# Kernel optimization log

Measured on AMD Instinct MI355X. Metric: run time of the kernel, lower is better.

## Reference

```python
import jax, jax.numpy as jnp
import numpy as np

H = 132  # hidden size hard-coded in SpatialRelationLayer

def _mlp(x, w1, b1, w2, b2, w3, b3):
    # FCBlock: 2 hidden layers of width 132 with ReLU, then linear out;
    # NNNet wraps it with sigmoid(out * 5)
    h = jax.nn.relu(x @ w1 + b1)
    h = jax.nn.relu(h @ w2 + b2)
    return jax.nn.sigmoid((h @ w3 + b3) * 5.0)

def _mlp_params(key, din, dout):
    k1, k2, k3 = jax.random.split(key, 3)
    def lin(k, i, o):
        kw, kb = jax.random.split(k)
        s = 1.0 / np.sqrt(i)
        return (jax.random.uniform(kw, (i, o), jnp.float32, -s, s),
                jax.random.uniform(kb, (o,), jnp.float32, -s, s))
    w1, b1 = lin(k1, din, H)
    w2, b2 = lin(k2, H, H)
    w3, b3 = lin(k3, H, dout)
    return w1, b1, w2, b2, w3, b3

def setup_inputs() -> dict:
    key = jax.random.key(0)
    b, N, D0, D1, D2 = 8, 128, 128, 128, 64
    O0, O1, O2 = 64, 64, 64
    kP, kQ, kR, kp, kq, kr = jax.random.split(key, 6)
    inp = {
        "P": jax.random.normal(kP, (b, D0), jnp.float32),
        "Q": jax.random.normal(kQ, (b, N, D1), jnp.float32),
        "R": jax.random.normal(kR, (b, N, N, D2), jnp.float32),
    }
    for name, k, din, dout in (("p", kp, D0 + D1, O0),
                               ("q", kq, D1 + D0 + 2 * D2, O1),
                               ("r", kr, D2 + 2 * D1, O2)):
        w1, b1, w2, b2, w3, b3 = _mlp_params(k, din, dout)
        inp.update({f"{name}_w1": w1, f"{name}_b1": b1,
                    f"{name}_w2": w2, f"{name}_b2": b2,
                    f"{name}_w3": w3, f"{name}_b3": b3})
    return inp

def reference(P, Q, R,
              p_w1, p_b1, p_w2, p_b2, p_w3, p_b3,
              q_w1, q_b1, q_w2, q_b2, q_w3, q_b3,
              r_w1, r_b1, r_w2, r_b2, r_w3, r_b3):
    b, N, D1 = Q.shape
    # P branch: global max over objects, concat with P
    P_inputs = jnp.concatenate([jnp.max(Q, axis=1), P], axis=1)  # [b, D1+D0]
    P_out = _mlp(P_inputs, p_w1, p_b1, p_w2, p_b2, p_w3, p_b3)
    # Q branch: broadcast P per-object, max-reduce relations over each axis
    P_exp = jnp.broadcast_to(P[:, None, :], (b, N, P.shape[1]))  # [b,N,D0]
    R_red0 = jnp.max(R, axis=1)  # [b,N,D2]
    R_red1 = jnp.max(R, axis=2)  # [b,N,D2]
    Q_inputs = jnp.concatenate([P_exp, Q, R_red0, R_red1], axis=2)
    Q_out = _mlp(Q_inputs, q_w1, q_b1, q_w2, q_b2, q_w3, q_b3)
    # R branch: pairwise broadcast of Q along both axes, concat with R
    Q0 = jnp.broadcast_to(Q[:, None, :, :], (b, N, N, D1))  # repeat along dim 1
    Q1 = jnp.broadcast_to(Q[:, :, None, :], (b, N, N, D1))  # repeat along dim 2
    R_inputs = jnp.concatenate([R, Q0, Q1], axis=-1)  # [b,N,N,D2+2*D1]
    R_out = _mlp(R_inputs, r_w1, r_b1, r_w2, r_b2, r_w3, r_b3)
    return (P_out, Q_out, R_out)
```

## Files before the change

kernel.cpp:

```cpp
#include <hip/hip_runtime.h>

typedef _Float16 f16;
typedef f16 f16x8 __attribute__((ext_vector_type(8)));
typedef f16 f16x4 __attribute__((ext_vector_type(4)));
typedef float f32x4 __attribute__((ext_vector_type(4)));

#define MFMA16(a, b, c) __builtin_amdgcn_mfma_f32_16x16x32_f16(a, b, c, 0, 0, 0)

#define OFF_RW1A 0
#define OFF_RW2  10240
#define OFF_RW3  35840
#define OFF_QW1  46080
#define OFF_QW2  87040
#define OFF_QW3  112640
#define OFF_PW1  122880
#define OFF_PW2  163840
#define OFF_PW3  189440
#define PACK_BYTES 399360

#define PREP_BLOCKS 2419

struct InPtrs { const float* p[21]; };

__device__ const int g_mSrc[9] = {15, 17, 19, 9, 11, 13, 3, 5, 7};
__device__ const int g_mK0[9]  = {0, 0, 0, 128, 0, 0, 0, 0, 0};
__device__ const int g_mK[9]   = {64, 132, 132, 256, 132, 132, 256, 132, 132};
__device__ const int g_mN[9]   = {132, 132, 64, 132, 132, 64, 132, 132, 64};
__device__ const int g_mNT[9]  = {10, 10, 4, 10, 10, 4, 10, 10, 4};
__device__ const int g_mDst[9] = {OFF_RW1A, OFF_RW2, OFF_RW3, OFF_QW1, OFF_QW2, OFF_QW3,
                                  OFF_PW1, OFF_PW2, OFF_PW3};
__device__ const int g_mBlk0[9] = {1024, 1029, 1042, 1047, 1067, 1080, 1085, 1105, 1118};

__global__ __launch_bounds__(256) void prep_kernel(InPtrs in, f16* __restrict__ wpk,
    float* __restrict__ c1, float* __restrict__ d1, float* __restrict__ e1q,
    float* __restrict__ qmax, float* __restrict__ red0, float* __restrict__ red1)
{
  __shared__ float sbuf[1024];
  const int mb = blockIdx.x, t = threadIdx.x;

  if (mb < 1024) {
    const int b = mb >> 7, j = mb & 127;
    const float* base = in.p[2] + (size_t)b * 128 * 8192 + (size_t)j * 64 + (t & 15) * 4;
    const int g = t >> 4;
    f32x4 mm[8];
    #pragma unroll
    for (int v = 0; v < 8; ++v)
      mm[v] = *(const f32x4*)(base + (size_t)(g + 16 * v) * 8192);
    #pragma unroll
    for (int s = 4; s > 0; s >>= 1)
      #pragma unroll
      for (int v = 0; v < 4; ++v)
        if (v < s) {
          mm[v][0] = fmaxf(mm[v][0], mm[v + s][0]);
          mm[v][1] = fmaxf(mm[v][1], mm[v + s][1]);
          mm[v][2] = fmaxf(mm[v][2], mm[v + s][2]);
          mm[v][3] = fmaxf(mm[v][3], mm[v + s][3]);
        }
    float* sr = sbuf + g * 64 + (t & 15) * 4;
    sr[0] = mm[0][0]; sr[1] = mm[0][1]; sr[2] = mm[0][2]; sr[3] = mm[0][3];
    __syncthreads();
    if (t < 64) {
      float m = sbuf[t];
      #pragma unroll
      for (int g2 = 1; g2 < 16; ++g2) m = fmaxf(m, sbuf[g2 * 64 + t]);
      red0[(size_t)mb * 64 + t] = m;
    }
  } else if (mb < 1123) {
    int mi = 8;
    while (mi > 0 && mb < g_mBlk0[mi]) --mi;
    const int NT = g_mNT[mi], K = g_mK[mi], N = g_mN[mi], K0 = g_mK0[mi];
    const int L = (mb - g_mBlk0[mi]) * 256 + t;
    const int lanes = ((K + 31) >> 5) * NT * 64;
    if (L < lanes) {
      const int lane = L & 63, tile = L >> 6;
      const int kk = tile / NT, nn = tile % NT;
      const float* src = in.p[g_mSrc[mi]];
      const int n = nn * 16 + (lane & 15);
      const int kb = kk * 32 + ((lane >> 4) << 3);
      f16x8 v;
      #pragma unroll
      for (int u = 0; u < 8; ++u) {
        const int k = kb + u;
        float f = (k < K && n < N) ? src[(size_t)(K0 + k) * N + n] : 0.f;
        v[u] = (f16)f;
      }
      *(f16x8*)(wpk + g_mDst[mi] + (size_t)L * 8) = v;
    }
  } else if (mb < 1131) {
    const int b = mb - 1123;
    const float* Qb = in.p[1] + (size_t)b * 128 * 128;
    const int d = t & 127, g = t >> 7;
    float m0 = -3.4e38f, m1 = m0, m2 = m0, m3 = m0;
    #pragma unroll
    for (int v = 0; v < 16; ++v) {
      const int i = g * 64 + v * 4;
      m0 = fmaxf(m0, Qb[(size_t)(i + 0) * 128 + d]);
      m1 = fmaxf(m1, Qb[(size_t)(i + 1) * 128 + d]);
      m2 = fmaxf(m2, Qb[(size_t)(i + 2) * 128 + d]);
      m3 = fmaxf(m3, Qb[(size_t)(i + 3) * 128 + d]);
    }
    sbuf[g * 128 + d] = fmaxf(fmaxf(m0, m1), fmaxf(m2, m3));
    __syncthreads();
    if (t < 128) qmax[b * 128 + t] = fmaxf(sbuf[t], sbuf[128 + t]);
  } else if (mb < 1139) {
    const int b = mb - 1131;
    const float* P = in.p[0]; const float* qw1 = in.p[9]; const float* qb1 = in.p[10];
    if (t < 160) {
      float a = 0.f;
      if (t < 132) {
        float a0 = 0.f, a1 = 0.f, a2 = 0.f, a3 = 0.f;
        for (int k = 0; k < 128; k += 4) {
          a0 += P[b * 128 + k + 0] * qw1[(size_t)(k + 0) * 132 + t];
          a1 += P[b * 128 + k + 1] * qw1[(size_t)(k + 1) * 132 + t];
          a2 += P[b * 128 + k + 2] * qw1[(size_t)(k + 2) * 132 + t];
          a3 += P[b * 128 + k + 3] * qw1[(size_t)(k + 3) * 132 + t];
        }
        a = qb1[t] + (a0 + a1) + (a2 + a3);
      }
      e1q[b * 160 + t] = a;
    }
  } else if (mb < 1395) {
    const int blk = mb - 1139;
    const float* Q = in.p[1]; const float* rw1 = in.p[15]; const float* rb1 = in.p[16];
    for (int o = t; o < 512; o += 256) sbuf[o] = Q[(size_t)blk * 512 + o];
    __syncthreads();
    if (t < 160) {
      float cc[4], dd[4];
      #pragma unroll
      for (int r = 0; r < 4; ++r) { cc[r] = 0.f; dd[r] = 0.f; }
      if (t < 132) {
        const float bb = rb1[t];
        #pragma unroll
        for (int r = 0; r < 4; ++r) cc[r] = bb;
        for (int k = 0; k < 128; ++k) {
          const float wc = rw1[(size_t)(192 + k) * 132 + t];
          const float wd = rw1[(size_t)(64 + k) * 132 + t];
          #pragma unroll
          for (int r = 0; r < 4; ++r) {
            cc[r] += sbuf[r * 128 + k] * wc;
            dd[r] += sbuf[r * 128 + k] * wd;
          }
        }
      }
      for (int r = 0; r < 4; ++r) {
        c1[(size_t)(blk * 4 + r) * 160 + t] = cc[r];
        d1[(size_t)(blk * 4 + r) * 160 + t] = dd[r];
      }
    }
  } else {
    const int blk = mb - 1395;
    const float* base = in.p[2] + (size_t)blk * 8192 + (t & 15) * 4;
    const int g = t >> 4;
    f32x4 mm[8];
    #pragma unroll
    for (int v = 0; v < 8; ++v)
      mm[v] = *(const f32x4*)(base + (size_t)(g + 16 * v) * 64);
    #pragma unroll
    for (int s = 4; s > 0; s >>= 1)
      #pragma unroll
      for (int v = 0; v < 4; ++v)
        if (v < s) {
          mm[v][0] = fmaxf(mm[v][0], mm[v + s][0]);
          mm[v][1] = fmaxf(mm[v][1], mm[v + s][1]);
          mm[v][2] = fmaxf(mm[v][2], mm[v + s][2]);
          mm[v][3] = fmaxf(mm[v][3], mm[v + s][3]);
        }
    float* sr = sbuf + g * 64 + (t & 15) * 4;
    sr[0] = mm[0][0]; sr[1] = mm[0][1]; sr[2] = mm[0][2]; sr[3] = mm[0][3];
    __syncthreads();
    if (t < 64) {
      float m = sbuf[t];
      #pragma unroll
      for (int g2 = 1; g2 < 16; ++g2) m = fmaxf(m, sbuf[g2 * 64 + t]);
      red1[(size_t)blk * 64 + t] = m;
    }
  }
}

__device__ __forceinline__ float sig5(float x) {
  return 1.f / (1.f + __expf(-5.f * x));
}

__global__ __launch_bounds__(256, 2) void fused_kernel(
    const float* __restrict__ R, const float* __restrict__ c1, const float* __restrict__ d1,
    const float* __restrict__ rb2, const float* __restrict__ rb3,
    const f16* __restrict__ wpk, float* __restrict__ outR,
    const float* __restrict__ P, const float* __restrict__ Q,
    const float* __restrict__ qb2, const float* __restrict__ qb3,
    const float* __restrict__ pb1, const float* __restrict__ pb2, const float* __restrict__ pb3,
    const float* __restrict__ e1q, const float* __restrict__ qmax,
    const float* __restrict__ red0, const float* __restrict__ red1,
    float* __restrict__ outP, float* __restrict__ outQ)
{
  __shared__ __align__(16) char pool[81920];
  const int blk = blockIdx.x;
  const int t = threadIdx.x, lane = t & 63, w = t >> 6;
  const int wm = w >> 1, wn = w & 1;
  const int lr = (lane >> 4) << 2;
  const int lc = lane & 15;
  const int lk = (lane >> 4) << 3;

  if (blk < 1024) {
    f16 (*Xr)[72]  = (f16(*)[72])pool;
    f16 (*Hs)[168] = (f16(*)[168])(pool + 18432);
    const int rbase = wm * 64, nbase = wn * 80;

    const float* Rb = R + (size_t)blk * 8192;
    #pragma unroll
    for (int v = 0; v < 8; ++v) {
      const int quad = v * 256 + t;
      const int j = quad >> 4, kq = quad & 15;
      f32x4 rv = *(const f32x4*)(Rb + (size_t)j * 64 + kq * 4);
      f16x4 hv;
      hv[0] = (f16)rv[0]; hv[1] = (f16)rv[1]; hv[2] = (f16)rv[2]; hv[3] = (f16)rv[3];
      *(f16x4*)(&Xr[j][kq * 4]) = hv;
    }

    const int b = blk >> 7;
    const float* c1r = c1 + (size_t)blk * 160;
    const float* d1b = d1 + (size_t)b * 128 * 160;
    f32x4 acc[4][5];
    f32x4 cvv[5];
    #pragma unroll
    for (int n5 = 0; n5 < 5; ++n5)
      cvv[n5] = *(const f32x4*)(c1r + nbase + n5 * 16 + lr);
    #pragma unroll
    for (int mi2 = 0; mi2 < 4; ++mi2) {
      const int j = rbase + mi2 * 16 + lc;
      #pragma unroll
      for (int n5 = 0; n5 < 5; ++n5) {
        f32x4 dv = *(const f32x4*)(d1b + (size_t)j * 160 + nbase + n5 * 16 + lr);
        acc[mi2][n5] = cvv[n5] + dv;
      }
    }
    __syncthreads();
    const f16x8* W1p = (const f16x8*)(wpk + OFF_RW1A);
    #pragma unroll
    for (int kk = 0; kk < 2; ++kk) {
      f16x8 a[4];
      #pragma unroll
      for (int mi2 = 0; mi2 < 4; ++mi2)
        a[mi2] = *(const f16x8*)(&Xr[rbase + mi2 * 16 + lc][kk * 32 + lk]);
      #pragma unroll
      for (int n5 = 0; n5 < 5; ++n5) {
        const f16x8 bf = W1p[(size_t)(kk * 10 + wn * 5 + n5) * 64 + lane];
        #pragma unroll
        for (int mi2 = 0; mi2 < 4; ++mi2)
          acc[mi2][n5] = MFMA16(bf, a[mi2], acc[mi2][n5]);
      }
    }
    #pragma unroll
    for (int mi2 = 0; mi2 < 4; ++mi2) {
      const int j = rbase + mi2 * 16 + lc;
      #pragma unroll
      for (int n5 = 0; n5 < 5; ++n5) {
        f16x4 hv;
        #pragma unroll
        for (int r = 0; r < 4; ++r) hv[r] = (f16)fmaxf(acc[mi2][n5][r], 0.f);
        *(f16x4*)(&Hs[j][nbase + n5 * 16 + lr]) = hv;
      }
    }
    __syncthreads();

    #pragma unroll
    for (int n5 = 0; n5 < 5; ++n5) {
      const int nb = nbase + n5 * 16 + lr;
      f32x4 bv = {0.f, 0.f, 0.f, 0.f};
      if (nb < 132) bv = *(const f32x4*)(rb2 + nb);
      #pragma unroll
      for (int mi2 = 0; mi2 < 4; ++mi2) acc[mi2][n5] = bv;
    }
    const f16x8* W2p = (const f16x8*)(wpk + OFF_RW2);
    #pragma unroll
    for (int kk = 0; kk < 5; ++kk) {
      f16x8 a[4];
      #pragma unroll
      for (int mi2 = 0; mi2 < 4; ++mi2)
        a[mi2] = *(const f16x8*)(&Hs[rbase + mi2 * 16 + lc][kk * 32 + lk]);
      #pragma unroll
      for (int n5 = 0; n5 < 5; ++n5) {
        const f16x8 bf = W2p[(size_t)(kk * 10 + wn * 5 + n5) * 64 + lane];
        #pragma unroll
        for (int mi2 = 0; mi2 < 4; ++mi2)
          acc[mi2][n5] = MFMA16(bf, a[mi2], acc[mi2][n5]);
      }
    }
    __syncthreads();
    #pragma unroll
    for (int mi2 = 0; mi2 < 4; ++mi2) {
      const int j = rbase + mi2 * 16 + lc;
      #pragma unroll
      for (int n5 = 0; n5 < 5; ++n5) {
        f16x4 hv;
        #pragma unroll
        for (int r = 0; r < 4; ++r) hv[r] = (f16)fmaxf(acc[mi2][n5][r], 0.f);
        *(f16x4*)(&Hs[j][nbase + n5 * 16 + lr]) = hv;
      }
    }
    __syncthreads();

    f32x4 acc3[4][2];
    const int n3base = wn * 32;
    #pragma unroll
    for (int n2 = 0; n2 < 2; ++n2) {
      f32x4 bv = *(const f32x4*)(rb3 + n3base + n2 * 16 + lr);
      #pragma unroll
      for (int mi2 = 0; mi2 < 4; ++mi2) acc3[mi2][n2] = bv;
    }
    const f16x8* W3p = (const f16x8*)(wpk + OFF_RW3);
    #pragma unroll
    for (int kk = 0; kk < 5; ++kk) {
      f16x8 a[4];
      #pragma unroll
      for (int mi2 = 0; mi2 < 4; ++mi2)
        a[mi2] = *(const f16x8*)(&Hs[rbase + mi2 * 16 + lc][kk * 32 + lk]);
      #pragma unroll
      for (int n2 = 0; n2 < 2; ++n2) {
        const f16x8 bf = W3p[(size_t)(kk * 4 + wn * 2 + n2) * 64 + lane];
        #pragma unroll
        for (int mi2 = 0; mi2 < 4; ++mi2)
          acc3[mi2][n2] = MFMA16(bf, a[mi2], acc3[mi2][n2]);
      }
    }
    float* Ro = outR + (size_t)blk * 8192;
    #pragma unroll
    for (int mi2 = 0; mi2 < 4; ++mi2) {
      const int j = rbase + mi2 * 16 + lc;
      #pragma unroll
      for (int n2 = 0; n2 < 2; ++n2) {
        f32x4 ov;
        #pragma unroll
        for (int r = 0; r < 4; ++r) ov[r] = sig5(acc3[mi2][n2][r]);
        *(f32x4*)(Ro + (size_t)j * 64 + n3base + n2 * 16 + lr) = ov;
      }
    }
  } else {
    f16 (*Xc)[72]  = (f16(*)[72])pool;
    f16 (*Hs2)[168] = (f16(*)[168])(pool + 9216);
    f16* Wb = (f16*)(pool + 30720);
    const int bs = blk - 1024;
    const bool isP = (bs == 16);
    const int rb = wm * 32;
    const int b = bs >> 1, x0 = (bs & 1) * 64;
    const f16* W1g = wpk + (isP ? OFF_PW1 : OFF_QW1);
    const f16* W2g = wpk + (isP ? OFF_PW2 : OFF_QW2);
    const f16* W3g = wpk + (isP ? OFF_PW3 : OFF_QW3);

    f32x4 acc[2][5];
    #pragma unroll
    for (int n5 = 0; n5 < 5; ++n5) {
      const int nb = wn * 80 + n5 * 16 + lr;
      f32x4 cv = {0.f, 0.f, 0.f, 0.f};
      if (isP) { if (nb < 132) cv = *(const f32x4*)(pb1 + nb); }
      else cv = *(const f32x4*)(e1q + b * 160 + nb);
      acc[0][n5] = cv; acc[1][n5] = cv;
    }

    for (int c = 0; c < 4; ++c) {
      if ((c & 1) == 0) {
        const int half = c >> 1;
        for (int idx = t; idx < 40 * 64; idx += 256) {
          const int f = idx >> 6, ln = idx & 63;
          *(f16x8*)(&Wb[f * 512 + ln * 8]) =
              *(const f16x8*)(W1g + (size_t)(half * 40 + f) * 512 + ln * 8);
        }
      }
      for (int o = t; o < 1024; o += 256) {
        const int rr = o >> 4, kq = o & 15;
        f32x4 v = {0.f, 0.f, 0.f, 0.f};
        if (isP) {
          if (rr < 8) {
            const float* s = (c < 2) ? (qmax + rr * 128 + c * 64) : (P + rr * 128 + (c - 2) * 64);
            v = *(const f32x4*)(s + kq * 4);
          }
        } else {
          const size_t rowg = (size_t)(b * 128 + x0 + rr);
          const float* s = (c < 2) ? (Q + rowg * 128 + c * 64)
                                   : (((c == 2) ? red0 : red1) + rowg * 64);
          v = *(const f32x4*)(s + kq * 4);
        }
        f16x4 hv;
        hv[0] = (f16)v[0]; hv[1] = (f16)v[1]; hv[2] = (f16)v[2]; hv[3] = (f16)v[3];
        *(f16x4*)(&Xc[rr][kq * 4]) = hv;
      }
      __syncthreads();
      #pragma unroll
      for (int kk = 0; kk < 2; ++kk) {
        f16x8 a[2];
        #pragma unroll
        for (int mi2 = 0; mi2 < 2; ++mi2)
          a[mi2] = *(const f16x8*)(&Xc[rb + mi2 * 16 + lc][kk * 32 + lk]);
        #pragma unroll
        for (int n5 = 0; n5 < 5; ++n5) {
          const int rel = ((c & 1) * 2 + kk) * 10 + wn * 5 + n5;
          const f16x8 bf = *(const f16x8*)(&Wb[rel * 512 + lane * 8]);
          #pragma unroll
          for (int mi2 = 0; mi2 < 2; ++mi2)
            acc[mi2][n5] = MFMA16(bf, a[mi2], acc[mi2][n5]);
        }
      }
      __syncthreads();
    }
    #pragma unroll
    for (int mi2 = 0; mi2 < 2; ++mi2) {
      const int j = rb + mi2 * 16 + lc;
      #pragma unroll
      for (int n5 = 0; n5 < 5; ++n5) {
        f16x4 hv;
        #pragma unroll
        for (int r = 0; r < 4; ++r) hv[r] = (f16)fmaxf(acc[mi2][n5][r], 0.f);
        *(f16x4*)(&Hs2[j][wn * 80 + n5 * 16 + lr]) = hv;
      }
    }
    for (int idx = t; idx < 50 * 64; idx += 256) {
      const int f = idx >> 6, ln = idx & 63;
      *(f16x8*)(&Wb[f * 512 + ln * 8]) = *(const f16x8*)(W2g + (size_t)f * 512 + ln * 8);
    }
    #pragma unroll
    for (int n5 = 0; n5 < 5; ++n5) {
      const int nb = wn * 80 + n5 * 16 + lr;
      f32x4 bv = {0.f, 0.f, 0.f, 0.f};
      if (nb < 132) bv = *(const f32x4*)((isP ? pb2 : qb2) + nb);
      acc[0][n5] = bv; acc[1][n5] = bv;
    }
    __syncthreads();
    #pragma unroll
    for (int kk = 0; kk < 5; ++kk) {
      f16x8 a[2];
      #pragma unroll
      for (int mi2 = 0; mi2 < 2; ++mi2)
        a[mi2] = *(const f16x8*)(&Hs2[rb + mi2 * 16 + lc][kk * 32 + lk]);
      #pragma unroll
      for (int n5 = 0; n5 < 5; ++n5) {
        const f16x8 bf = *(const f16x8*)(&Wb[(kk * 10 + wn * 5 + n5) * 512 + lane * 8]);
        #pragma unroll
        for (int mi2 = 0; mi2 < 2; ++mi2)
          acc[mi2][n5] = MFMA16(bf, a[mi2], acc[mi2][n5]);
      }
    }
    __syncthreads();
    #pragma unroll
    for (int mi2 = 0; mi2 < 2; ++mi2) {
      const int j = rb + mi2 * 16 + lc;
      #pragma unroll
      for (int n5 = 0; n5 < 5; ++n5) {
        f16x4 hv;
        #pragma unroll
        for (int r = 0; r < 4; ++r) hv[r] = (f16)fmaxf(acc[mi2][n5][r], 0.f);
        *(f16x4*)(&Hs2[j][wn * 80 + n5 * 16 + lr]) = hv;
      }
    }
    for (int idx = t; idx < 20 * 64; idx += 256) {
      const int f = idx >> 6, ln = idx & 63;
      *(f16x8*)(&Wb[f * 512 + ln * 8]) = *(const f16x8*)(W3g + (size_t)f * 512 + ln * 8);
    }
    __syncthreads();

    f32x4 acc3[2][2];
    const int n3base = wn * 32;
    #pragma unroll
    for (int n2 = 0; n2 < 2; ++n2) {
      f32x4 bv = *(const f32x4*)((isP ? pb3 : qb3) + n3base + n2 * 16 + lr);
      acc3[0][n2] = bv; acc3[1][n2] = bv;
    }
    #pragma unroll
    for (int kk = 0; kk < 5; ++kk) {
      f16x8 a[2];
      #pragma unroll
      for (int mi2 = 0; mi2 < 2; ++mi2)
        a[mi2] = *(const f16x8*)(&Hs2[rb + mi2 * 16 + lc][kk * 32 + lk]);
      #pragma unroll
      for (int n2 = 0; n2 < 2; ++n2) {
        const f16x8 bf = *(const f16x8*)(&Wb[(kk * 4 + wn * 2 + n2) * 512 + lane * 8]);
        #pragma unroll
        for (int mi2 = 0; mi2 < 2; ++mi2)
          acc3[mi2][n2] = MFMA16(bf, a[mi2], acc3[mi2][n2]);
      }
    }
    #pragma unroll
    for (int mi2 = 0; mi2 < 2; ++mi2) {
      const int j = rb + mi2 * 16 + lc;
      #pragma unroll
      for (int n2 = 0; n2 < 2; ++n2) {
        f32x4 ov;
        #pragma unroll
        for (int r = 0; r < 4; ++r) ov[r] = sig5(acc3[mi2][n2][r]);
        if (isP) {
          if (j < 8) *(f32x4*)(outP + (size_t)j * 64 + n3base + n2 * 16 + lr) = ov;
        } else {
          *(f32x4*)(outQ + ((size_t)(b * 128 + x0 + j)) * 64 + n3base + n2 * 16 + lr) = ov;
        }
      }
    }
  }
}

extern "C" void kernel_launch(void* const* d_in, const int* in_sizes, int n_in,
                              void* d_out, int out_size, void* d_ws, size_t ws_size,
                              hipStream_t stream) {
  (void)in_sizes; (void)n_in; (void)out_size; (void)ws_size;
  InPtrs ip;
  for (int i = 0; i < 21; ++i) ip.p[i] = (const float*)d_in[i];

  char* ws = (char*)d_ws;
  f16* wpk = (f16*)ws;
  float* wsf = (float*)(ws + PACK_BYTES);
  float* c1 = wsf;
  float* d1 = wsf + 163840;
  float* e1q = wsf + 327680;
  float* qmax = wsf + 328960;
  float* red0 = wsf + 329984;
  float* red1 = wsf + 395520;

  float* outP = (float*)d_out;
  float* outQ = outP + 512;
  float* outR = outP + 66048;

  prep_kernel<<<dim3(PREP_BLOCKS), dim3(256), 0, stream>>>(ip, wpk, c1, d1, e1q, qmax, red0, red1);
  fused_kernel<<<dim3(1041), dim3(256), 0, stream>>>((const float*)d_in[2], c1, d1,
      (const float*)d_in[18], (const float*)d_in[20], wpk, outR,
      (const float*)d_in[0], (const float*)d_in[1],
      (const float*)d_in[12], (const float*)d_in[14],
      (const float*)d_in[4], (const float*)d_in[6], (const float*)d_in[8],
      e1q, qmax, red0, red1, outP, outQ);
}
```

Baseline: 73.55 us.

## Halve R-block tile, load MLP inputs directly to registers, restructure max reductions

The fused kernel now handles 64 rows per block instead of 128, doubling the grid and cutting shared memory to a single hidden-state buffer so launch bounds rise to 4 blocks per SM. Input fragments (R, Q, reductions) are loaded from global memory and converted to f16 in registers instead of being staged through LDS, and weights are read directly from global memory rather than being copied into shared buffers. The prep kernel's red0 and red1 reductions are rewritten with fewer blocks, each looping over more rows with 2-wide loads, which shrinks the prep grid. The intent is higher occupancy and fewer barriers and LDS round trips, at the cost of redundant global weight reads per block and less reuse of each weight fragment across rows.

```diff
diff --git a/kernel.cpp b/kernel.cpp
--- a/kernel.cpp
+++ b/kernel.cpp
@@ -4,6 +4,7 @@
 typedef f16 f16x8 __attribute__((ext_vector_type(8)));
 typedef f16 f16x4 __attribute__((ext_vector_type(4)));
 typedef float f32x4 __attribute__((ext_vector_type(4)));
+typedef float f32x2 __attribute__((ext_vector_type(2)));
 
 #define MFMA16(a, b, c) __builtin_amdgcn_mfma_f32_16x16x32_f16(a, b, c, 0, 0, 0)
 
@@ -18,7 +19,7 @@
 #define OFF_PW3  189440
 #define PACK_BYTES 399360
 
-#define PREP_BLOCKS 2419
+#define PREP_BLOCKS 1523
 
 struct InPtrs { const float* p[21]; };
 
@@ -29,7 +30,7 @@
 __device__ const int g_mNT[9]  = {10, 10, 4, 10, 10, 4, 10, 10, 4};
 __device__ const int g_mDst[9] = {OFF_RW1A, OFF_RW2, OFF_RW3, OFF_QW1, OFF_QW2, OFF_QW3,
                                   OFF_PW1, OFF_PW2, OFF_PW3};
-__device__ const int g_mBlk0[9] = {1024, 1029, 1042, 1047, 1067, 1080, 1085, 1105, 1118};
+__device__ const int g_mBlk0[9] = {128, 133, 146, 151, 171, 184, 189, 209, 222};
 
 __global__ __launch_bounds__(256) void prep_kernel(InPtrs in, f16* __restrict__ wpk,
     float* __restrict__ c1, float* __restrict__ d1, float* __restrict__ e1q,
@@ -38,34 +39,30 @@
   __shared__ float sbuf[1024];
   const int mb = blockIdx.x, t = threadIdx.x;
 
-  if (mb < 1024) {
-    const int b = mb >> 7, j = mb & 127;
-    const float* base = in.p[2] + (size_t)b * 128 * 8192 + (size_t)j * 64 + (t & 15) * 4;
-    const int g = t >> 4;
-    f32x4 mm[8];
-    #pragma unroll
-    for (int v = 0; v < 8; ++v)
-      mm[v] = *(const f32x4*)(base + (size_t)(g + 16 * v) * 8192);
+  if (mb < 128) {
+    const int b = mb >> 4, jo = mb & 15;
+    const float* base = in.p[2] + (size_t)b * 1048576 + (size_t)jo * 512 + t * 2;
+    f32x2 m[8];
+    #pragma unroll
+    for (int u = 0; u < 8; ++u) { m[u][0] = -3.4e38f; m[u][1] = -3.4e38f; }
+    for (int i = 0; i < 128; i += 8) {
+      #pragma unroll
+      for (int u = 0; u < 8; ++u) {
+        f32x2 v = *(const f32x2*)(base + (size_t)(i + u) * 8192);
+        m[u][0] = fmaxf(m[u][0], v[0]);
+        m[u][1] = fmaxf(m[u][1], v[1]);
+      }
+    }
     #pragma unroll
     for (int s = 4; s > 0; s >>= 1)
       #pragma unroll
-      for (int v = 0; v < 4; ++v)
-        if (v < s) {
-          mm[v][0] = fmaxf(mm[v][0], mm[v + s][0]);
-          mm[v][1] = fmaxf(mm[v][1], mm[v + s][1]);
-          mm[v][2] = fmaxf(mm[v][2], mm[v + s][2]);
-          mm[v][3] = fmaxf(mm[v][3], mm[v + s][3]);
+      for (int u = 0; u < 4; ++u)
+        if (u < s) {
+          m[u][0] = fmaxf(m[u][0], m[u + s][0]);
+          m[u][1] = fmaxf(m[u][1], m[u + s][1]);
         }
-    float* sr = sbuf + g * 64 + (t & 15) * 4;
-    sr[0] = mm[0][0]; sr[1] = mm[0][1]; sr[2] = mm[0][2]; sr[3] = mm[0][3];
-    __syncthreads();
-    if (t < 64) {
-      float m = sbuf[t];
-      #pragma unroll
-      for (int g2 = 1; g2 < 16; ++g2) m = fmaxf(m, sbuf[g2 * 64 + t]);
-      red0[(size_t)mb * 64 + t] = m;
-    }
-  } else if (mb < 1123) {
+    *(f32x2*)(red0 + ((size_t)(b * 128 + jo * 8 + (t >> 5))) * 64 + ((t * 2) & 63)) = m[0];
+  } else if (mb < 227) {
     int mi = 8;
     while (mi > 0 && mb < g_mBlk0[mi]) --mi;
     const int NT = g_mNT[mi], K = g_mK[mi], N = g_mN[mi], K0 = g_mK0[mi];
@@ -86,8 +83,8 @@
       }
       *(f16x8*)(wpk + g_mDst[mi] + (size_t)L * 8) = v;
     }
-  } else if (mb < 1131) {
-    const int b = mb - 1123;
+  } else if (mb < 235) {
+    const int b = mb - 227;
     const float* Qb = in.p[1] + (size_t)b * 128 * 128;
     const int d = t & 127, g = t >> 7;
     float m0 = -3.4e38f, m1 = m0, m2 = m0, m3 = m0;
@@ -102,8 +99,8 @@
     sbuf[g * 128 + d] = fmaxf(fmaxf(m0, m1), fmaxf(m2, m3));
     __syncthreads();
     if (t < 128) qmax[b * 128 + t] = fmaxf(sbuf[t], sbuf[128 + t]);
-  } else if (mb < 1139) {
-    const int b = mb - 1131;
+  } else if (mb < 243) {
+    const int b = mb - 235;
     const float* P = in.p[0]; const float* qw1 = in.p[9]; const float* qb1 = in.p[10];
     if (t < 160) {
       float a = 0.f;
@@ -119,8 +116,8 @@
       }
       e1q[b * 160 + t] = a;
     }
-  } else if (mb < 1395) {
-    const int blk = mb - 1139;
+  } else if (mb < 499) {
+    const int blk = mb - 243;
     const float* Q = in.p[1]; const float* rw1 = in.p[15]; const float* rb1 = in.p[16];
     for (int o = t; o < 512; o += 256) sbuf[o] = Q[(size_t)blk * 512 + o];
     __syncthreads();
@@ -148,31 +145,31 @@
       }
     }
   } else {
-    const int blk = mb - 1395;
-    const float* base = in.p[2] + (size_t)blk * 8192 + (t & 15) * 4;
-    const int g = t >> 4;
-    f32x4 mm[8];
-    #pragma unroll
-    for (int v = 0; v < 8; ++v)
-      mm[v] = *(const f32x4*)(base + (size_t)(g + 16 * v) * 64);
-    #pragma unroll
-    for (int s = 4; s > 0; s >>= 1)
-      #pragma unroll
-      for (int v = 0; v < 4; ++v)
-        if (v < s) {
-          mm[v][0] = fmaxf(mm[v][0], mm[v + s][0]);
-          mm[v][1] = fmaxf(mm[v][1], mm[v + s][1]);
-          mm[v][2] = fmaxf(mm[v][2], mm[v + s][2]);
-          mm[v][3] = fmaxf(mm[v][3], mm[v + s][3]);
-        }
-    float* sr = sbuf + g * 64 + (t & 15) * 4;
-    sr[0] = mm[0][0]; sr[1] = mm[0][1]; sr[2] = mm[0][2]; sr[3] = mm[0][3];
+    const int bi = mb - 499;
+    const int d2 = t & 31, jg = t >> 5;
+    const float* base = in.p[2] + (size_t)bi * 8192 + (size_t)jg * 1024 + d2 * 2;
+    f32x2 m[4];
+    #pragma unroll
+    for (int u = 0; u < 4; ++u) { m[u][0] = -3.4e38f; m[u][1] = -3.4e38f; }
+    #pragma unroll
+    for (int v = 0; v < 16; v += 4) {
+      #pragma unroll
+      for (int u = 0; u < 4; ++u) {
+        f32x2 vv = *(const f32x2*)(base + (size_t)(v + u) * 64);
+        m[u][0] = fmaxf(m[u][0], vv[0]);
+        m[u][1] = fmaxf(m[u][1], vv[1]);
+      }
+    }
+    m[0][0] = fmaxf(fmaxf(m[0][0], m[1][0]), fmaxf(m[2][0], m[3][0]));
+    m[0][1] = fmaxf(fmaxf(m[0][1], m[1][1]), fmaxf(m[2][1], m[3][1]));
+    sbuf[jg * 64 + d2 * 2] = m[0][0];
+    sbuf[jg * 64 + d2 * 2 + 1] = m[0][1];
     __syncthreads();
     if (t < 64) {
-      float m = sbuf[t];
-      #pragma unroll
-      for (int g2 = 1; g2 < 16; ++g2) m = fmaxf(m, sbuf[g2 * 64 + t]);
-      red1[(size_t)blk * 64 + t] = m;
+      float mm = sbuf[t];
+      #pragma unroll
+      for (int g2 = 1; g2 < 8; ++g2) mm = fmaxf(mm, sbuf[g2 * 64 + t]);
+      red1[(size_t)bi * 64 + t] = mm;
     }
   }
 }
@@ -181,7 +178,16 @@
   return 1.f / (1.f + __expf(-5.f * x));
 }
 
-__global__ __launch_bounds__(256, 2) void fused_kernel(
+__device__ __forceinline__ f16x8 ld_frag_f32(const float* p) {
+  f32x4 v0 = *(const f32x4*)(p);
+  f32x4 v1 = *(const f32x4*)(p + 4);
+  f16x8 a;
+  a[0] = (f16)v0[0]; a[1] = (f16)v0[1]; a[2] = (f16)v0[2]; a[3] = (f16)v0[3];
+  a[4] = (f16)v1[0]; a[5] = (f16)v1[1]; a[6] = (f16)v1[2]; a[7] = (f16)v1[3];
+  return a;
+}
+
+__global__ __launch_bounds__(256, 4) void fused_kernel(
     const float* __restrict__ R, const float* __restrict__ c1, const float* __restrict__ d1,
     const float* __restrict__ rb2, const float* __restrict__ rb3,
     const f16* __restrict__ wpk, float* __restrict__ outR,
@@ -192,304 +198,191 @@
     const float* __restrict__ red0, const float* __restrict__ red1,
     float* __restrict__ outP, float* __restrict__ outQ)
 {
-  __shared__ __align__(16) char pool[81920];
+  __shared__ f16 Hs[64][168];
   const int blk = blockIdx.x;
   const int t = threadIdx.x, lane = t & 63, w = t >> 6;
   const int wm = w >> 1, wn = w & 1;
   const int lr = (lane >> 4) << 2;
   const int lc = lane & 15;
   const int lk = (lane >> 4) << 3;
-
-  if (blk < 1024) {
-    f16 (*Xr)[72]  = (f16(*)[72])pool;
-    f16 (*Hs)[168] = (f16(*)[168])(pool + 18432);
-    const int rbase = wm * 64, nbase = wn * 80;
-
-    const float* Rb = R + (size_t)blk * 8192;
-    #pragma unroll
-    for (int v = 0; v < 8; ++v) {
-      const int quad = v * 256 + t;
-      const int j = quad >> 4, kq = quad & 15;
-      f32x4 rv = *(const f32x4*)(Rb + (size_t)j * 64 + kq * 4);
-      f16x4 hv;
-      hv[0] = (f16)rv[0]; hv[1] = (f16)rv[1]; hv[2] = (f16)rv[2]; hv[3] = (f16)rv[3];
-      *(f16x4*)(&Xr[j][kq * 4]) = hv;
-    }
-
-    const int b = blk >> 7;
-    const float* c1r = c1 + (size_t)blk * 160;
-    const float* d1b = d1 + (size_t)b * 128 * 160;
-    f32x4 acc[4][5];
+  const int rbase = wm * 32, nbase = wn * 80;
+
+  f32x4 acc[2][5];
+  const float* b2p;
+  const float* b3p;
+  const f16x8* W2p;
+  const f16x8* W3p;
+  float* obase;
+  int rowlim;
+
+  if (blk >= 17) {
+    const int idx = blk - 17;
+    const int bi = idx >> 1, half = idx & 1;
+    const int jbase = half * 64;
+    const int b = bi >> 7;
+    const float* Rb = R + (size_t)bi * 8192 + (size_t)jbase * 64;
+
+    const float* c1r = c1 + (size_t)bi * 160;
+    const float* d1b = d1 + ((size_t)b * 128 + jbase) * 160;
     f32x4 cvv[5];
     #pragma unroll
     for (int n5 = 0; n5 < 5; ++n5)
       cvv[n5] = *(const f32x4*)(c1r + nbase + n5 * 16 + lr);
     #pragma unroll
-    for (int mi2 = 0; mi2 < 4; ++mi2) {
-      const int j = rbase + mi2 * 16 + lc;
-      #pragma unroll
-      for (int n5 = 0; n5 < 5; ++n5) {
-        f32x4 dv = *(const f32x4*)(d1b + (size_t)j * 160 + nbase + n5 * 16 + lr);
-        acc[mi2][n5] = cvv[n5] + dv;
-      }
-    }
-    __syncthreads();
+    for (int mi2 = 0; mi2 < 2; ++mi2) {
+      const int jl = rbase + mi2 * 16 + lc;
+      const float* dr = d1b + (size_t)jl * 160 + nbase + lr;
+      #pragma unroll
+      for (int n5 = 0; n5 < 5; ++n5)
+        acc[mi2][n5] = cvv[n5] + *(const f32x4*)(dr + n5 * 16);
+    }
     const f16x8* W1p = (const f16x8*)(wpk + OFF_RW1A);
     #pragma unroll
     for (int kk = 0; kk < 2; ++kk) {
-      f16x8 a[4];
-      #pragma unroll
-      for (int mi2 = 0; mi2 < 4; ++mi2)
-        a[mi2] = *(const f16x8*)(&Xr[rbase + mi2 * 16 + lc][kk * 32 + lk]);
+      const f16x8 a0 = ld_frag_f32(Rb + (size_t)(rbase + lc) * 64 + kk * 32 + lk);
+      const f16x8 a1 = ld_frag_f32(Rb + (size_t)(rbase + 16 + lc) * 64 + kk * 32 + lk);
       #pragma unroll
       for (int n5 = 0; n5 < 5; ++n5) {
         const f16x8 bf = W1p[(size_t)(kk * 10 + wn * 5 + n5) * 64 + lane];
-        #pragma unroll
-        for (int mi2 = 0; mi2 < 4; ++mi2)
-          acc[mi2][n5] = MFMA16(bf, a[mi2], acc[mi2][n5]);
-      }
-    }
-    #pragma unroll
-    for (int mi2 = 0; mi2 < 4; ++mi2) {
-      const int j = rbase + mi2 * 16 + lc;
-      #pragma unroll
-      for (int n5 = 0; n5 < 5; ++n5) {
-        f16x4 hv;
-        #pragma unroll
-        for (int r = 0; r < 4; ++r) hv[r] = (f16)fmaxf(acc[mi2][n5][r], 0.f);
-        *(f16x4*)(&Hs[j][nbase + n5 * 16 + lr]) = hv;
-      }
-    }
-    __syncthreads();
+        acc[0][n5] = MFMA16(bf, a0, acc[0][n5]);
+        acc[1][n5] = MFMA16(bf, a1, acc[1][n5]);
+      }
+    }
+    b2p = rb2; b3p = rb3;
+    W2p = (const f16x8*)(wpk + OFF_RW2);
+    W3p = (const f16x8*)(wpk + OFF_RW3);
+    obase = outR + (size_t)bi * 8192 + (size_t)jbase * 64;
+    rowlim = 64;
+  } else {
+    const int bs = blk;
+    const bool isP = (bs == 16);
+    const int b = bs >> 1, x0 = (bs & 1) * 64;
+    const f16x8* W1p = (const f16x8*)(wpk + (isP ? OFF_PW1 : OFF_QW1));
+    const f16x8 zz = {0, 0, 0, 0, 0, 0, 0, 0};
 
     #pragma unroll
     for (int n5 = 0; n5 < 5; ++n5) {
       const int nb = nbase + n5 * 16 + lr;
-      f32x4 bv = {0.f, 0.f, 0.f, 0.f};
-      if (nb < 132) bv = *(const f32x4*)(rb2 + nb);
-      #pragma unroll
-      for (int mi2 = 0; mi2 < 4; ++mi2) acc[mi2][n5] = bv;
-    }
-    const f16x8* W2p = (const f16x8*)(wpk + OFF_RW2);
-    #pragma unroll
-    for (int kk = 0; kk < 5; ++kk) {
-      f16x8 a[4];
-      #pragma unroll
-      for (int mi2 = 0; mi2 < 4; ++mi2)
-        a[mi2] = *(const f16x8*)(&Hs[rbase + mi2 * 16 + lc][kk * 32 + lk]);
-      #pragma unroll
-      for (int n5 = 0; n5 < 5; ++n5) {
-        const f16x8 bf = W2p[(size_t)(kk * 10 + wn * 5 + n5) * 64 + lane];
+      f32x4 cv = {0.f, 0.f, 0.f, 0.f};
+      if (isP) { if (nb < 132) cv = *(const f32x4*)(pb1 + nb); }
+      else cv = *(const f32x4*)(e1q + b * 160 + nb);
+      acc[0][n5] = cv; acc[1][n5] = cv;
+    }
+    for (int c = 0; c < 4; ++c) {
+      #pragma unroll
+      for (int kk = 0; kk < 2; ++kk) {
+        const int kq = c * 64 + kk * 32 + lk;
+        f16x8 a0 = zz, a1 = zz;
+        if (isP) {
+          #pragma unroll
+          for (int mi2 = 0; mi2 < 2; ++mi2) {
+            const int rl = rbase + mi2 * 16 + lc;
+            f16x8 av = zz;
+            if (rl < 8) {
+              const float* s = (c < 2) ? (qmax + rl * 128 + kq) : (P + rl * 128 + (kq - 128));
+              av = ld_frag_f32(s);
+            }
+            if (mi2 == 0) a0 = av; else a1 = av;
+          }
+        } else {
+          #pragma unroll
+          for (int mi2 = 0; mi2 < 2; ++mi2) {
+            const size_t rg = (size_t)(b * 128 + x0 + rbase + mi2 * 16 + lc);
+            const float* s = (c < 2) ? (Q + rg * 128 + kq)
+                           : ((kq < 192) ? (red0 + rg * 64 + (kq - 128))
+                                         : (red1 + rg * 64 + (kq - 192)));
+            const f16x8 av = ld_frag_f32(s);
+            if (mi2 == 0) a0 = av; else a1 = av;
+          }
+        }
         #pragma unroll
-        for (int mi2 = 0; mi2 < 4; ++mi2)
-          acc[mi2][n5] = MFMA16(bf, a[mi2], acc[mi2][n5]);
-      }
-    }
-    __syncthreads();
-    #pragma unroll
-    for (int mi2 = 0; mi2 < 4; ++mi2) {
-      const int j = rbase + mi2 * 16 + lc;
-      #pragma unroll
-      for (int n5 = 0; n5 < 5; ++n5) {
-        f16x4 hv;
-        #pragma unroll
-        for (int r = 0; r < 4; ++r) hv[r] = (f16)fmaxf(acc[mi2][n5][r], 0.f);
-        *(f16x4*)(&Hs[j][nbase + n5 * 16 + lr]) = hv;
-      }
-    }
-    __syncthreads();
-
-    f32x4 acc3[4][2];
-    const int n3base = wn * 32;
+        for (int n5 = 0; n5 < 5; ++n5) {
+          const f16x8 bf = W1p[(size_t)((c * 2 + kk) * 10 + wn * 5 + n5) * 64 + lane];
+          acc[0][n5] = MFMA16(bf, a0, acc[0][n5]);
+          acc[1][n5] = MFMA16(bf, a1, acc[1][n5]);
+        }
+      }
+    }
+    b2p = isP ? pb2 : qb2; b3p = isP ? pb3 : qb3;
+    W2p = (const f16x8*)(wpk + (isP ? OFF_PW2 : OFF_QW2));
+    W3p = (const f16x8*)(wpk + (isP ? OFF_PW3 : OFF_QW3));
+    obase = isP ? outP : (outQ + ((size_t)(b * 128 + x0)) * 64);
+    rowlim = isP ? 8 : 64;
+  }
+
+  #pragma unroll
+  for (int mi2 = 0; mi2 < 2; ++mi2) {
+    const int jl = rbase + mi2 * 16 + lc;
+    #pragma unroll
+    for (int n5 = 0; n5 < 5; ++n5) {
+      f16x4 hv;
+      #pragma unroll
+      for (int r = 0; r < 4; ++r) hv[r] = (f16)fmaxf(acc[mi2][n5][r], 0.f);
+      *(f16x4*)(&Hs[jl][nbase + n5 * 16 + lr]) = hv;
+    }
+  }
+  __syncthreads();
+
+  #pragma unroll
+  for (int n5 = 0; n5 < 5; ++n5) {
+    const int nb = nbase + n5 * 16 + lr;
+    f32x4 bv = {0.f, 0.f, 0.f, 0.f};
+    if (nb < 132) bv = *(const f32x4*)(b2p + nb);
+    acc[0][n5] = bv; acc[1][n5] = bv;
+  }
+  #pragma unroll
+  for (int kk = 0; kk < 5; ++kk) {
+    const f16x8 a0 = *(const f16x8*)(&Hs[rbase + lc][kk * 32 + lk]);
+    const f16x8 a1 = *(const f16x8*)(&Hs[rbase + 16 + lc][kk * 32 + lk]);
+    #pragma unroll
+    for (int n5 = 0; n5 < 5; ++n5) {
+      const f16x8 bf = W2p[(size_t)(kk * 10 + wn * 5 + n5) * 64 + lane];
+      acc[0][n5] = MFMA16(bf, a0, acc[0][n5]);
+      acc[1][n5] = MFMA16(bf, a1, acc[1][n5]);
+    }
+  }
+  __syncthreads();
+  #pragma unroll
+  for (int mi2 = 0; mi2 < 2; ++mi2) {
+    const int jl = rbase + mi2 * 16 + lc;
+    #pragma unroll
+    for (int n5 = 0; n5 < 5; ++n5) {
+      f16x4 hv;
+      #pragma unroll
+      for (int r = 0; r < 4; ++r) hv[r] = (f16)fmaxf(acc[mi2][n5][r], 0.f);
+      *(f16x4*)(&Hs[jl][nbase + n5 * 16 + lr]) = hv;
+    }
+  }
+  __syncthreads();
+
+  f32x4 acc3[2][2];
+  const int n3base = wn * 32;
+  #pragma unroll
+  for (int n2 = 0; n2 < 2; ++n2) {
+    const f32x4 bv = *(const f32x4*)(b3p + n3base + n2 * 16 + lr);
+    acc3[0][n2] = bv; acc3[1][n2] = bv;
+  }
+  #pragma unroll
+  for (int kk = 0; kk < 5; ++kk) {
+    const f16x8 a0 = *(const f16x8*)(&Hs[rbase + lc][kk * 32 + lk]);
+    const f16x8 a1 = *(const f16x8*)(&Hs[rbase + 16 + lc][kk * 32 + lk]);
     #pragma unroll
     for (int n2 = 0; n2 < 2; ++n2) {
-      f32x4 bv = *(const f32x4*)(rb3 + n3base + n2 * 16 + lr);
-      #pragma unroll
-      for (int mi2 = 0; mi2 < 4; ++mi2) acc3[mi2][n2] = bv;
-    }
-    const f16x8* W3p = (const f16x8*)(wpk + OFF_RW3);
-    #pragma unroll
-    for (int kk = 0; kk < 5; ++kk) {
-      f16x8 a[4];
-      #pragma unroll
-      for (int mi2 = 0; mi2 < 4; ++mi2)
-        a[mi2] = *(const f16x8*)(&Hs[rbase + mi2 * 16 + lc][kk * 32 + lk]);
-      #pragma unroll
-      for (int n2 = 0; n2 < 2; ++n2) {
-        const f16x8 bf = W3p[(size_t)(kk * 4 + wn * 2 + n2) * 64 + lane];
-        #pragma unroll
-        for (int mi2 = 0; mi2 < 4; ++mi2)
-          acc3[mi2][n2] = MFMA16(bf, a[mi2], acc3[mi2][n2]);
-      }
-    }
-    float* Ro = outR + (size_t)blk * 8192;
-    #pragma unroll
-    for (int mi2 = 0; mi2 < 4; ++mi2) {
-      const int j = rbase + mi2 * 16 + lc;
+      const f16x8 bf = W3p[(size_t)(kk * 4 + wn * 2 + n2) * 64 + lane];
+      acc3[0][n2] = MFMA16(bf, a0, acc3[0][n2]);
+      acc3[1][n2] = MFMA16(bf, a1, acc3[1][n2]);
+    }
+  }
+  #pragma unroll
+  for (int mi2 = 0; mi2 < 2; ++mi2) {
+    const int jl = rbase + mi2 * 16 + lc;
+    if (jl < rowlim) {
       #pragma unroll
       for (int n2 = 0; n2 < 2; ++n2) {
         f32x4 ov;
         #pragma unroll
         for (int r = 0; r < 4; ++r) ov[r] = sig5(acc3[mi2][n2][r]);
-        *(f32x4*)(Ro + (size_t)j * 64 + n3base + n2 * 16 + lr) = ov;
-      }
-    }
-  } else {
-    f16 (*Xc)[72]  = (f16(*)[72])pool;
-    f16 (*Hs2)[168] = (f16(*)[168])(pool + 9216);
-    f16* Wb = (f16*)(pool + 30720);
-    const int bs = blk - 1024;
-    const bool isP = (bs == 16);
-    const int rb = wm * 32;
-    const int b = bs >> 1, x0 = (bs & 1) * 64;
-    const f16* W1g = wpk + (isP ? OFF_PW1 : OFF_QW1);
-    const f16* W2g = wpk + (isP ? OFF_PW2 : OFF_QW2);
-    const f16* W3g = wpk + (isP ? OFF_PW3 : OFF_QW3);
-
-    f32x4 acc[2][5];
-    #pragma unroll
-    for (int n5 = 0; n5 < 5; ++n5) {
-      const int nb = wn * 80 + n5 * 16 + lr;
-      f32x4 cv = {0.f, 0.f, 0.f, 0.f};
-      if (isP) { if (nb < 132) cv = *(const f32x4*)(pb1 + nb); }
-      else cv = *(const f32x4*)(e1q + b * 160 + nb);
-      acc[0][n5] = cv; acc[1][n5] = cv;
-    }
-
-    for (int c = 0; c < 4; ++c) {
-      if ((c & 1) == 0) {
-        const int half = c >> 1;
-        for (int idx = t; idx < 40 * 64; idx += 256) {
-          const int f = idx >> 6, ln = idx & 63;
-          *(f16x8*)(&Wb[f * 512 + ln * 8]) =
-              *(const f16x8*)(W1g + (size_t)(half * 40 + f) * 512 + ln * 8);
-        }
-      }
-      for (int o = t; o < 1024; o += 256) {
-        const int rr = o >> 4, kq = o & 15;
-        f32x4 v = {0.f, 0.f, 0.f, 0.f};
-        if (isP) {
-          if (rr < 8) {
-            const float* s = (c < 2) ? (qmax + rr * 128 + c * 64) : (P + rr * 128 + (c - 2) * 64);
-            v = *(const f32x4*)(s + kq * 4);
-          }
-        } else {
-          const size_t rowg = (size_t)(b * 128 + x0 + rr);
-          const float* s = (c < 2) ? (Q + rowg * 128 + c * 64)
-                                   : (((c == 2) ? red0 : red1) + rowg * 64);
-          v = *(const f32x4*)(s + kq * 4);
-        }
-        f16x4 hv;
-        hv[0] = (f16)v[0]; hv[1] = (f16)v[1]; hv[2] = (f16)v[2]; hv[3] = (f16)v[3];
-        *(f16x4*)(&Xc[rr][kq * 4]) = hv;
-      }
-      __syncthreads();
-      #pragma unroll
-      for (int kk = 0; kk < 2; ++kk) {
-        f16x8 a[2];
-        #pragma unroll
-        for (int mi2 = 0; mi2 < 2; ++mi2)
-          a[mi2] = *(const f16x8*)(&Xc[rb + mi2 * 16 + lc][kk * 32 + lk]);
-        #pragma unroll
-        for (int n5 = 0; n5 < 5; ++n5) {
-          const int rel = ((c & 1) * 2 + kk) * 10 + wn * 5 + n5;
-          const f16x8 bf = *(const f16x8*)(&Wb[rel * 512 + lane * 8]);
-          #pragma unroll
-          for (int mi2 = 0; mi2 < 2; ++mi2)
-            acc[mi2][n5] = MFMA16(bf, a[mi2], acc[mi2][n5]);
-        }
-      }
-      __syncthreads();
-    }
-    #pragma unroll
-    for (int mi2 = 0; mi2 < 2; ++mi2) {
-      const int j = rb + mi2 * 16 + lc;
-      #pragma unroll
-      for (int n5 = 0; n5 < 5; ++n5) {
-        f16x4 hv;
-        #pragma unroll
-        for (int r = 0; r < 4; ++r) hv[r] = (f16)fmaxf(acc[mi2][n5][r], 0.f);
-        *(f16x4*)(&Hs2[j][wn * 80 + n5 * 16 + lr]) = hv;
-      }
-    }
-    for (int idx = t; idx < 50 * 64; idx += 256) {
-      const int f = idx >> 6, ln = idx & 63;
-      *(f16x8*)(&Wb[f * 512 + ln * 8]) = *(const f16x8*)(W2g + (size_t)f * 512 + ln * 8);
-    }
-    #pragma unroll
-    for (int n5 = 0; n5 < 5; ++n5) {
-      const int nb = wn * 80 + n5 * 16 + lr;
-      f32x4 bv = {0.f, 0.f, 0.f, 0.f};
-      if (nb < 132) bv = *(const f32x4*)((isP ? pb2 : qb2) + nb);
-      acc[0][n5] = bv; acc[1][n5] = bv;
-    }
-    __syncthreads();
-    #pragma unroll
-    for (int kk = 0; kk < 5; ++kk) {
-      f16x8 a[2];
-      #pragma unroll
-      for (int mi2 = 0; mi2 < 2; ++mi2)
-        a[mi2] = *(const f16x8*)(&Hs2[rb + mi2 * 16 + lc][kk * 32 + lk]);
-      #pragma unroll
-      for (int n5 = 0; n5 < 5; ++n5) {
-        const f16x8 bf = *(const f16x8*)(&Wb[(kk * 10 + wn * 5 + n5) * 512 + lane * 8]);
-        #pragma unroll
-        for (int mi2 = 0; mi2 < 2; ++mi2)
-          acc[mi2][n5] = MFMA16(bf, a[mi2], acc[mi2][n5]);
-      }
-    }
-    __syncthreads();
-    #pragma unroll
-    for (int mi2 = 0; mi2 < 2; ++mi2) {
-      const int j = rb + mi2 * 16 + lc;
-      #pragma unroll
-      for (int n5 = 0; n5 < 5; ++n5) {
-        f16x4 hv;
-        #pragma unroll
-        for (int r = 0; r < 4; ++r) hv[r] = (f16)fmaxf(acc[mi2][n5][r], 0.f);
-        *(f16x4*)(&Hs2[j][wn * 80 + n5 * 16 + lr]) = hv;
-      }
-    }
-    for (int idx = t; idx < 20 * 64; idx += 256) {
-      const int f = idx >> 6, ln = idx & 63;
-      *(f16x8*)(&Wb[f * 512 + ln * 8]) = *(const f16x8*)(W3g + (size_t)f * 512 + ln * 8);
-    }
-    __syncthreads();
-
-    f32x4 acc3[2][2];
-    const int n3base = wn * 32;
-    #pragma unroll
-    for (int n2 = 0; n2 < 2; ++n2) {
-      f32x4 bv = *(const f32x4*)((isP ? pb3 : qb3) + n3base + n2 * 16 + lr);
-      acc3[0][n2] = bv; acc3[1][n2] = bv;
-    }
-    #pragma unroll
-    for (int kk = 0; kk < 5; ++kk) {
-      f16x8 a[2];
-      #pragma unroll
-      for (int mi2 = 0; mi2 < 2; ++mi2)
-        a[mi2] = *(const f16x8*)(&Hs2[rb + mi2 * 16 + lc][kk * 32 + lk]);
-      #pragma unroll
-      for (int n2 = 0; n2 < 2; ++n2) {
-        const f16x8 bf = *(const f16x8*)(&Wb[(kk * 4 + wn * 2 + n2) * 512 + lane * 8]);
-        #pragma unroll
-        for (int mi2 = 0; mi2 < 2; ++mi2)
-          acc3[mi2][n2] = MFMA16(bf, a[mi2], acc3[mi2][n2]);
-      }
-    }
-    #pragma unroll
-    for (int mi2 = 0; mi2 < 2; ++mi2) {
-      const int j = rb + mi2 * 16 + lc;
-      #pragma unroll
-      for (int n2 = 0; n2 < 2; ++n2) {
-        f32x4 ov;
-        #pragma unroll
-        for (int r = 0; r < 4; ++r) ov[r] = sig5(acc3[mi2][n2][r]);
-        if (isP) {
-          if (j < 8) *(f32x4*)(outP + (size_t)j * 64 + n3base + n2 * 16 + lr) = ov;
-        } else {
-          *(f32x4*)(outQ + ((size_t)(b * 128 + x0 + j)) * 64 + n3base + n2 * 16 + lr) = ov;
-        }
+        *(f32x4*)(obase + (size_t)jl * 64 + n3base + n2 * 16 + lr) = ov;
       }
     }
   }
@@ -517,7 +410,7 @@
   float* outR = outP + 66048;
 
   prep_kernel<<<dim3(PREP_BLOCKS), dim3(256), 0, stream>>>(ip, wpk, c1, d1, e1q, qmax, red0, red1);
-  fused_kernel<<<dim3(1041), dim3(256), 0, stream>>>((const float*)d_in[2], c1, d1,
+  fused_kernel<<<dim3(2065), dim3(256), 0, stream>>>((const float*)d_in[2], c1, d1,
       (const float*)d_in[18], (const float*)d_in[20], wpk, outR,
       (const float*)d_in[0], (const float*)d_in[1],
       (const float*)d_in[12], (const float*)d_in[14],
```

After: 64.46 us. -12.4%, faster.
